# Performance work log

Measured on AMD Instinct MI355X. Metric: run time of the kernel, lower is better.

The kernel has to match this reference:

```python
import jax, jax.numpy as jnp
import numpy as np

# Qwen2 MoE MLP layer: top-k router -> token dispatch -> grouped SwiGLU MLP -> weighted combine.
S, B, H = 2048, 1, 1024      # seq, batch, hidden
E, K, F = 8, 2, 1408         # num_experts, top_k, moe_intermediate (fc1 emits 2*F for SwiGLU)

def setup_inputs() -> dict:
    key = jax.random.key(0)
    k1, k2, k3, k4 = jax.random.split(key, 4)
    return {
        "hidden_states": jax.random.normal(k1, (S, B, H), jnp.float32),
        "router_weight": jax.random.normal(k2, (H, E), jnp.float32) * 0.02,
        "w1": jax.random.normal(k3, (E, H, 2 * F), jnp.float32) * 0.02,  # grouped fc1 (gate|up)
        "w2": jax.random.normal(k4, (E, F, H), jnp.float32) * 0.02,      # grouped fc2
    }

def reference(hidden_states, router_weight, w1, w2):
    s, b, h = hidden_states.shape
    x = hidden_states.reshape(-1, h)                      # [T, H], T = S*B
    logits = x @ router_weight                            # [T, E]
    probs = jax.nn.softmax(logits, axis=-1)
    _, topk_idx = jax.lax.top_k(probs, K)                 # token -> top-k expert ids
    routing_map = jax.nn.one_hot(topk_idx, E, dtype=probs.dtype).sum(axis=1)  # [T, E] 0/1 mask
    local_probs = probs * routing_map                     # combine weights, zero off-topk
    # Grouped SwiGLU MLP. The torch module permutes tokens to expert groups and runs
    # grouped GEMMs; with static shapes the equivalent math is dense-per-expert with
    # the routing mask folded into the combine weights (identical output).
    y = jnp.einsum('th,ehf->tef', x, w1)                  # [T, E, 2F]
    y1, y2 = jnp.split(y, 2, axis=-1)
    g = jax.nn.silu(y1) * y2                              # swiglu, [T, E, F]
    o = jnp.einsum('tef,efh->teh', g, w2)                 # [T, E, H]
    out = jnp.einsum('teh,te->th', o, local_probs)        # unpermute + prob-weighted combine
    return out.reshape(s, b, h)
```

## Files before the change

kernel.cpp:

```cpp
#include <hip/hip_runtime.h>
#include <hip/hip_bf16.h>
#include <stdint.h>

#define T_TOK 2048
#define HD    1024
#define NE    8
#define FD    1408
#define F2D   2816
#define HP    1056
#define OP    1056

#define BM 128
#define BK 32
#define MAXMT 40
#define MAXSLOTS 5120
#define FC1_NT 22
#define FC2_NT 16
#define FC1_NWG (FC1_NT * MAXMT)
#define FC2_NWG (FC2_NT * MAXMT)
#define FC1_CHUNK 110
#define FC2_CHUNK 80

typedef __attribute__((ext_vector_type(8))) short bf16x8;
typedef __attribute__((ext_vector_type(4))) float f32x4;
typedef __attribute__((ext_vector_type(2))) int i32x2;

__device__ __forceinline__ unsigned short f2bf(float f) {
  unsigned int u = __float_as_uint(f);
  u += 0x7FFFu + ((u >> 16) & 1u);
  return (unsigned short)(u >> 16);
}

#define GLL16(gp, lp) __builtin_amdgcn_global_load_lds( \
    (const __attribute__((address_space(1))) void*)(gp), \
    (__attribute__((address_space(3))) void*)(lp), 16, 0, 0)

#define LDS_OFF(p) ((unsigned)(uintptr_t)(__attribute__((address_space(3))) const unsigned short*)(p))

__device__ __forceinline__ void tr_issue(unsigned a, i32x2& lo, i32x2& hi) {
  asm volatile("ds_read_b64_tr_b16 %0, %2\n\t"
               "ds_read_b64_tr_b16 %1, %2 offset:512"
               : "=&v"(lo), "=&v"(hi)
               : "v"(a)
               : "memory");
}
__device__ __forceinline__ bf16x8 tr_pack(i32x2 lo, i32x2 hi) {
  union { i32x2 v; short s[4]; } a, b;
  a.v = lo; b.v = hi;
  bf16x8 f;
  f[0] = a.s[0]; f[1] = a.s[1]; f[2] = a.s[2]; f[3] = a.s[3];
  f[4] = b.s[0]; f[5] = b.s[1]; f[6] = b.s[2]; f[7] = b.s[3];
  return f;
}

__global__ __launch_bounds__(256) void k_router(
    const float* __restrict__ x, const float* __restrict__ rw,
    unsigned short* __restrict__ xbf, int* __restrict__ ctrl,
    int* __restrict__ tok_e, float* __restrict__ tok_p)
{
  const int lane = threadIdx.x & 63;
  const int t = blockIdx.x * 4 + (threadIdx.x >> 6);
  const float* xr = x + (size_t)t * HD;

  float part[8];
#pragma unroll
  for (int e = 0; e < 8; ++e) part[e] = 0.f;

#pragma unroll
  for (int i = 0; i < 16; ++i) {
    const int h = i * 64 + lane;
    const float xv = xr[h];
    xbf[(size_t)t * HP + h] = f2bf(xv);
    const float4* rwr = reinterpret_cast<const float4*>(rw + (size_t)h * 8);
    float4 a = rwr[0], bb = rwr[1];
    part[0] += xv * a.x; part[1] += xv * a.y; part[2] += xv * a.z; part[3] += xv * a.w;
    part[4] += xv * bb.x; part[5] += xv * bb.y; part[6] += xv * bb.z; part[7] += xv * bb.w;
  }
#pragma unroll
  for (int e = 0; e < 8; ++e) {
    float v = part[e];
#pragma unroll
    for (int d = 32; d; d >>= 1) v += __shfl_xor(v, d, 64);
    part[e] = v;
  }
  float m = part[0];
#pragma unroll
  for (int e = 1; e < 8; ++e) m = fmaxf(m, part[e]);
  float p[8], s = 0.f;
#pragma unroll
  for (int e = 0; e < 8; ++e) { p[e] = __expf(part[e] - m); s += p[e]; }
  const float inv = 1.f / s;
#pragma unroll
  for (int e = 0; e < 8; ++e) p[e] *= inv;

  int e0 = 0; float p0 = p[0];
#pragma unroll
  for (int e = 1; e < 8; ++e) if (p[e] > p0) { p0 = p[e]; e0 = e; }
  int e1 = -1; float p1 = -1.f;
#pragma unroll
  for (int e = 0; e < 8; ++e) if (e != e0 && p[e] > p1) { p1 = p[e]; e1 = e; }

  if (lane == 0) {
    tok_e[t * 2 + 0] = e0; tok_e[t * 2 + 1] = e1;
    tok_p[t * 2 + 0] = p0; tok_p[t * 2 + 1] = p1;
    atomicAdd(&ctrl[e0], 1);
    atomicAdd(&ctrl[e1], 1);
  }
}

__global__ __launch_bounds__(256) void k_offsets(
    int* __restrict__ ctrl, int* __restrict__ stok, float* __restrict__ sp,
    int* __restrict__ widmt1, int* __restrict__ widmt2)
{
  __shared__ int soff[8], scnt[8], sFirst[8], sNmt[8], sTake[8];
  __shared__ int sSpill;
  if (threadIdx.x == 0) {
    int o = 0, nm = 0, spill = 0;
    for (int e = 0; e < 8; ++e) {
      ctrl[16 + e] = o; soff[e] = o; scnt[e] = ctrl[e];
      const int n = ctrl[e];
      const int nmt = (n + BM - 1) / BM;
      sFirst[e] = nm; sNmt[e] = nmt; sTake[e] = nmt < 5 ? nmt : 5;
      if (nmt > 5) spill = 1;
      for (int j = 0; j < nmt; ++j) { ctrl[24 + nm] = e; ctrl[64 + nm] = o + j * BM; ++nm; }
      o += nmt * BM;
    }
    for (int i = nm; i < MAXMT; ++i) ctrl[24 + i] = -1;
    sSpill = spill;
  }
  __syncthreads();
  for (int i = threadIdx.x; i < FC1_NWG; i += 256) {
    const int e = i / FC1_CHUNK, r = i % FC1_CHUNK;
    const int j = r / FC1_NT, n = r % FC1_NT;
    widmt1[i] = (j < sTake[e]) ? (sFirst[e] + j) * 32 + n : -1;
  }
  for (int i = threadIdx.x; i < FC2_NWG; i += 256) {
    const int e = i / FC2_CHUNK, r = i % FC2_CHUNK;
    const int j = r / FC2_NT, n = r % FC2_NT;
    widmt2[i] = (j < sTake[e]) ? (sFirst[e] + j) * 32 + n : -1;
  }
  __syncthreads();
  if (sSpill && threadIdx.x == 0) {
    int cur = 0;
    for (int e = 0; e < 8; ++e)
      for (int j = 5; j < sNmt[e]; ++j)
        for (int n = 0; n < FC1_NT; ++n) {
          while (widmt1[cur] != -1) ++cur;
          widmt1[cur] = (sFirst[e] + j) * 32 + n;
        }
    cur = 0;
    for (int e = 0; e < 8; ++e)
      for (int j = 5; j < sNmt[e]; ++j)
        for (int n = 0; n < FC2_NT; ++n) {
          while (widmt2[cur] != -1) ++cur;
          widmt2[cur] = (sFirst[e] + j) * 32 + n;
        }
  }
  for (int e = 0; e < 8; ++e) {
    const int n = scnt[e], o = soff[e];
    const int padEnd = (n + BM - 1) / BM * BM;
    for (int j = n + (int)threadIdx.x; j < padEnd; j += 256) {
      stok[o + j] = 0; sp[o + j] = 0.f;
    }
  }
}

__global__ __launch_bounds__(256) void k_scatter(
    int* __restrict__ ctrl, const int* __restrict__ tok_e,
    const float* __restrict__ tok_p, int* __restrict__ stok,
    float* __restrict__ sp, int* __restrict__ tslot)
{
  const int t = blockIdx.x * 256 + threadIdx.x;
#pragma unroll
  for (int k = 0; k < 2; ++k) {
    const int e = tok_e[t * 2 + k];
    const float pp = tok_p[t * 2 + k];
    const int pos = atomicAdd(&ctrl[8 + e], 1);
    const int slot = ctrl[16 + e] + pos;
    stok[slot] = t; sp[slot] = pp;
    tslot[t * 2 + k] = slot;
  }
}

__global__ __launch_bounds__(256) void k_fc1(
    const unsigned short* __restrict__ xbf,
    const float* __restrict__ w1,
    const int* __restrict__ ctrl,
    const int* __restrict__ stok,
    const float* __restrict__ sp,
    const int* __restrict__ widmt1,
    unsigned short* __restrict__ g)
{
  const int bid = blockIdx.x;
  const int wid = (bid & 7) * FC1_CHUNK + (bid >> 3);
  const int packed = widmt1[wid];
  if (packed < 0) return;
  const int mt = packed >> 5;
  const int e = ctrl[24 + mt];
  const int rowbase = ctrl[64 + mt];
  const int n0 = (packed & 31) * 64;

  __shared__ unsigned short sA[3][BM * BK];
  __shared__ unsigned short sB1[3][64 * BK];
  __shared__ unsigned short sB2[3][64 * BK];

  const int tid = threadIdx.x;
  const int lane = tid & 63;
  const int wave = tid >> 6;
  const int wm = wave >> 1, wn = wave & 1;

  const int schunk = (lane & 3) ^ ((lane >> 3) & 3);
  const unsigned short* aSrc[2];
#pragma unroll
  for (int t4 = 0; t4 < 2; ++t4) {
    const int row = (t4 * 4 + wave) * 16 + (lane >> 2);
    const int tok = stok[rowbase + row];
    aSrc[t4] = xbf + (size_t)tok * HP + schunk * 8;
  }

  const int kdec = wave * 8 + ((lane >> 5) << 2) + ((lane >> 1) & 3);
  const int ndec = ((lane >> 3) & 3) * 16 + (lane & 1) * 8;
  const float* b1SrcF = w1 + ((size_t)e * HD + kdec) * F2D + n0 + ndec;
  const float* b2SrcF = b1SrcF + FD;

  const int c = lane >> 4;
  int aoff[4];
#pragma unroll
  for (int m = 0; m < 4; ++m) {
    const int row = wm * 64 + m * 16 + (lane & 15);
    aoff[m] = row * 32 + ((c ^ ((row >> 1) & 3)) << 3);
  }
  const unsigned trlane = (lane & 15) * 8 + (lane >> 4) * 1024;
  unsigned trb[2];
#pragma unroll
  for (int n = 0; n < 2; ++n) trb[n] = trlane + (wn * 2 + n) * 128;
  const unsigned b1base = LDS_OFF(&sB1[0][0]);
  const unsigned b2base = LDS_OFF(&sB2[0][0]);

  const f32x4 zero = {0.f, 0.f, 0.f, 0.f};
  f32x4 acc1[4][2], acc2[4][2];
#pragma unroll
  for (int m = 0; m < 4; ++m)
#pragma unroll
    for (int n = 0; n < 2; ++n) { acc1[m][n] = zero; acc2[m][n] = zero; }

  float b1r0[8], b2r0[8], b1r1[8], b2r1[8];

#define FC1_BLOAD(KT, R1, R2) do {                                  \
    const float* _p1 = b1SrcF + (size_t)(KT) * BK * F2D;            \
    const float* _p2 = b2SrcF + (size_t)(KT) * BK * F2D;            \
    *(float4*)&R1[0] = *(const float4*)_p1;                         \
    *(float4*)&R1[4] = *(const float4*)(_p1 + 4);                   \
    *(float4*)&R2[0] = *(const float4*)_p2;                         \
    *(float4*)&R2[4] = *(const float4*)(_p2 + 4);                   \
  } while (0)

#define FC1_BWRITE(BUF, R1, R2) do {                                \
    bf16x8 _v1, _v2;                                                \
    for (int _j = 0; _j < 8; ++_j) {                                \
      _v1[_j] = (short)f2bf(R1[_j]);                                \
      _v2[_j] = (short)f2bf(R2[_j]);                                \
    }                                                               \
    *(bf16x8*)&sB1[BUF][wave * 512 + lane * 8] = _v1;               \
    *(bf16x8*)&sB2[BUF][wave * 512 + lane * 8] = _v2;               \
  } while (0)

#define FC1_ASTAGE(BUF, KT) do {                                    \
    for (int _t4 = 0; _t4 < 2; ++_t4)                               \
      GLL16(aSrc[_t4] + (size_t)(KT) * BK, &sA[BUF][(_t4 * 4 + wave) * 512]); \
  } while (0)

  const int NSTEP = HD / BK;
  FC1_BLOAD(0, b1r0, b2r0);
  __builtin_amdgcn_sched_barrier(0);
  asm volatile("s_waitcnt vmcnt(0)" ::: "memory");
  FC1_BWRITE(0, b1r0, b2r0);
  __builtin_amdgcn_sched_barrier(0);
  FC1_BLOAD(1, b1r1, b2r1);
  __builtin_amdgcn_sched_barrier(0);
  FC1_ASTAGE(0, 0);
  __builtin_amdgcn_sched_barrier(0);
  FC1_BLOAD(2, b1r0, b2r0);
  __builtin_amdgcn_sched_barrier(0);
  FC1_ASTAGE(1, 1);
  __builtin_amdgcn_sched_barrier(0);
  asm volatile("s_waitcnt lgkmcnt(0)" ::: "memory");

#define FC1_STEP(T, R1, R2) do {                                             \
    const int _t = (T);                                                      \
    if (_t < NSTEP - 2)      { asm volatile("s_waitcnt vmcnt(6)" ::: "memory"); } \
    else if (_t == NSTEP - 2){ asm volatile("s_waitcnt vmcnt(2)" ::: "memory"); } \
    else                     { asm volatile("s_waitcnt vmcnt(0)" ::: "memory"); } \
    __builtin_amdgcn_s_barrier();                                            \
    __builtin_amdgcn_sched_barrier(0);                                       \
    int _bnext = bsel + 1; if (_bnext >= 3) _bnext -= 3;                     \
    int _bn2 = bsel + 2; if (_bn2 >= 3) _bn2 -= 3;                           \
    if (_t + 1 < NSTEP) FC1_BWRITE(_bnext, R1, R2);                          \
    __builtin_amdgcn_sched_barrier(0);                                       \
    if (_t + 3 < NSTEP) FC1_BLOAD(_t + 3, R1, R2);                           \
    __builtin_amdgcn_sched_barrier(0);                                       \
    if (_t + 2 < NSTEP) FC1_ASTAGE(_bn2, _t + 2);                            \
    __builtin_amdgcn_sched_barrier(0);                                       \
    bf16x8 _af[4];                                                           \
    for (int _m = 0; _m < 4; ++_m)                                           \
      _af[_m] = *(const bf16x8*)&sA[bsel][aoff[_m]];                         \
    i32x2 _q1lo[2], _q1hi[2], _q2lo[2], _q2hi[2];                            \
    for (int _n = 0; _n < 2; ++_n) {                                         \
      tr_issue(b1base + bsel * 4096 + trb[_n], _q1lo[_n], _q1hi[_n]);        \
      tr_issue(b2base + bsel * 4096 + trb[_n], _q2lo[_n], _q2hi[_n]);        \
    }                                                                        \
    asm volatile("s_waitcnt lgkmcnt(0)" ::: "memory");                       \
    __builtin_amdgcn_sched_barrier(0);                                       \
    bf16x8 _b1f[2], _b2f[2];                                                 \
    for (int _n = 0; _n < 2; ++_n) {                                         \
      _b1f[_n] = tr_pack(_q1lo[_n], _q1hi[_n]);                              \
      _b2f[_n] = tr_pack(_q2lo[_n], _q2hi[_n]);                              \
    }                                                                        \
    __builtin_amdgcn_s_setprio(1);                                           \
    for (int _m = 0; _m < 4; ++_m)                                           \
      for (int _n = 0; _n < 2; ++_n) {                                       \
        acc1[_m][_n] = __builtin_amdgcn_mfma_f32_16x16x32_bf16(_af[_m], _b1f[_n], acc1[_m][_n], 0, 0, 0); \
        acc2[_m][_n] = __builtin_amdgcn_mfma_f32_16x16x32_bf16(_af[_m], _b2f[_n], acc2[_m][_n], 0, 0, 0); \
      }                                                                      \
    __builtin_amdgcn_s_setprio(0);                                           \
  } while (0)

  int bsel = 0;
  for (int tt = 0; tt < NSTEP; tt += 2) {
    FC1_STEP(tt, b1r1, b2r1);
    bsel = bsel + 1 == 3 ? 0 : bsel + 1;
    FC1_STEP(tt + 1, b1r0, b2r0);
    bsel = bsel + 1 == 3 ? 0 : bsel + 1;
  }

  float prv[4][4];
#pragma unroll
  for (int m = 0; m < 4; ++m)
#pragma unroll
    for (int r = 0; r < 4; ++r)
      prv[m][r] = sp[rowbase + wm * 64 + m * 16 + (lane >> 4) * 4 + r];

#pragma unroll
  for (int m = 0; m < 4; ++m) {
    const int rb = rowbase + wm * 64 + m * 16 + (lane >> 4) * 4;
#pragma unroll
    for (int n = 0; n < 2; ++n) {
      const int col = n0 + wn * 32 + n * 16 + (lane & 15);
#pragma unroll
      for (int r = 0; r < 4; ++r) {
        const float y1 = acc1[m][n][r];
        const float y2 = acc2[m][n][r];
        const float gv = y1 / (1.f + __expf(-y1)) * y2 * prv[m][r];
        g[(size_t)(rb + r) * FD + col] = f2bf(gv);
      }
    }
  }
}

__global__ __launch_bounds__(256) void k_fc2(
    const unsigned short* __restrict__ g,
    const float* __restrict__ w2,
    const int* __restrict__ ctrl,
    const int* __restrict__ widmt2,
    float* __restrict__ o)
{
  const int bid = blockIdx.x;
  const int wid = (bid & 7) * FC2_CHUNK + (bid >> 3);
  const int packed = widmt2[wid];
  if (packed < 0) return;
  const int mt = packed >> 5;
  const int e = ctrl[24 + mt];
  const int rowbase = ctrl[64 + mt];
  const int n0 = (packed & 31) * 64;

  __shared__ unsigned short sA[3][BM * BK];
  __shared__ unsigned short sB[3][64 * BK];

  const int tid = threadIdx.x;
  const int lane = tid & 63;
  const int wave = tid >> 6;
  const int wm = wave >> 1, wn = wave & 1;

  const int schunk = (lane & 3) ^ ((lane >> 3) & 3);
  const unsigned short* aSrc[2];
#pragma unroll
  for (int t4 = 0; t4 < 2; ++t4) {
    const int row = (t4 * 4 + wave) * 16 + (lane >> 2);
    aSrc[t4] = g + (size_t)(rowbase + row) * FD + schunk * 8;
  }

  const int kdec = wave * 8 + ((lane >> 5) << 2) + ((lane >> 1) & 3);
  const int ndec = ((lane >> 3) & 3) * 16 + (lane & 1) * 8;
  const float* bSrcF = w2 + ((size_t)e * FD + kdec) * HD + n0 + ndec;

  const int c = lane >> 4;
  int aoff[4];
#pragma unroll
  for (int m = 0; m < 4; ++m) {
    const int row = wm * 64 + m * 16 + (lane & 15);
    aoff[m] = row * 32 + ((c ^ ((row >> 1) & 3)) << 3);
  }
  const unsigned trlane = (lane & 15) * 8 + (lane >> 4) * 1024;
  unsigned trb[2];
#pragma unroll
  for (int n = 0; n < 2; ++n) trb[n] = trlane + (wn * 2 + n) * 128;
  const unsigned bbase = LDS_OFF(&sB[0][0]);

  const f32x4 zero = {0.f, 0.f, 0.f, 0.f};
  f32x4 acc[4][2];
#pragma unroll
  for (int m = 0; m < 4; ++m)
#pragma unroll
    for (int n = 0; n < 2; ++n) acc[m][n] = zero;

  float br0[8], br1[8];

#define FC2_BLOAD(KT, R) do {                                       \
    const float* _p = bSrcF + (size_t)(KT) * BK * HD;               \
    *(float4*)&R[0] = *(const float4*)_p;                           \
    *(float4*)&R[4] = *(const float4*)(_p + 4);                     \
  } while (0)

#define FC2_BWRITE(BUF, R) do {                                     \
    bf16x8 _v;                                                      \
    for (int _j = 0; _j < 8; ++_j) _v[_j] = (short)f2bf(R[_j]);     \
    *(bf16x8*)&sB[BUF][wave * 512 + lane * 8] = _v;                 \
  } while (0)

#define FC2_ASTAGE(BUF, KT) do {                                    \
    for (int _t4 = 0; _t4 < 2; ++_t4)                               \
      GLL16(aSrc[_t4] + (size_t)(KT) * BK, &sA[BUF][(_t4 * 4 + wave) * 512]); \
  } while (0)

  const int NSTEP = FD / BK;
  FC2_BLOAD(0, br0);
  __builtin_amdgcn_sched_barrier(0);
  asm volatile("s_waitcnt vmcnt(0)" ::: "memory");
  FC2_BWRITE(0, br0);
  __builtin_amdgcn_sched_barrier(0);
  FC2_BLOAD(1, br1);
  __builtin_amdgcn_sched_barrier(0);
  FC2_ASTAGE(0, 0);
  __builtin_amdgcn_sched_barrier(0);
  FC2_BLOAD(2, br0);
  __builtin_amdgcn_sched_barrier(0);
  FC2_ASTAGE(1, 1);
  __builtin_amdgcn_sched_barrier(0);
  asm volatile("s_waitcnt lgkmcnt(0)" ::: "memory");

#define FC2_STEP(T, R) do {                                                  \
    const int _t = (T);                                                      \
    if (_t < NSTEP - 2)      { asm volatile("s_waitcnt vmcnt(4)" ::: "memory"); } \
    else if (_t == NSTEP - 2){ asm volatile("s_waitcnt vmcnt(2)" ::: "memory"); } \
    else                     { asm volatile("s_waitcnt vmcnt(0)" ::: "memory"); } \
    __builtin_amdgcn_s_barrier();                                            \
    __builtin_amdgcn_sched_barrier(0);                                       \
    int _bnext = bsel + 1; if (_bnext >= 3) _bnext -= 3;                     \
    int _bn2 = bsel + 2; if (_bn2 >= 3) _bn2 -= 3;                           \
    if (_t + 1 < NSTEP) FC2_BWRITE(_bnext, R);                               \
    __builtin_amdgcn_sched_barrier(0);                                       \
    if (_t + 3 < NSTEP) FC2_BLOAD(_t + 3, R);                                \
    __builtin_amdgcn_sched_barrier(0);                                       \
    if (_t + 2 < NSTEP) FC2_ASTAGE(_bn2, _t + 2);                            \
    __builtin_amdgcn_sched_barrier(0);                                       \
    bf16x8 _af[4];                                                           \
    for (int _m = 0; _m < 4; ++_m)                                           \
      _af[_m] = *(const bf16x8*)&sA[bsel][aoff[_m]];                         \
    i32x2 _qlo[2], _qhi[2];                                                  \
    for (int _n = 0; _n < 2; ++_n)                                           \
      tr_issue(bbase + bsel * 4096 + trb[_n], _qlo[_n], _qhi[_n]);           \
    asm volatile("s_waitcnt lgkmcnt(0)" ::: "memory");                       \
    __builtin_amdgcn_sched_barrier(0);                                       \
    bf16x8 _bf[2];                                                           \
    for (int _n = 0; _n < 2; ++_n) _bf[_n] = tr_pack(_qlo[_n], _qhi[_n]);    \
    __builtin_amdgcn_s_setprio(1);                                           \
    for (int _m = 0; _m < 4; ++_m)                                           \
      for (int _n = 0; _n < 2; ++_n)                                         \
        acc[_m][_n] = __builtin_amdgcn_mfma_f32_16x16x32_bf16(_af[_m], _bf[_n], acc[_m][_n], 0, 0, 0); \
    __builtin_amdgcn_s_setprio(0);                                           \
  } while (0)

  int bsel = 0;
  for (int tt = 0; tt < NSTEP; tt += 2) {
    FC2_STEP(tt, br1);
    bsel = bsel + 1 == 3 ? 0 : bsel + 1;
    FC2_STEP(tt + 1, br0);
    bsel = bsel + 1 == 3 ? 0 : bsel + 1;
  }

#pragma unroll
  for (int m = 0; m < 4; ++m) {
    const int rb = rowbase + wm * 64 + m * 16 + (lane >> 4) * 4;
#pragma unroll
    for (int n = 0; n < 2; ++n) {
      const int col = n0 + wn * 32 + n * 16 + (lane & 15);
#pragma unroll
      for (int r = 0; r < 4; ++r)
        o[(size_t)(rb + r) * OP + col] = acc[m][n][r];
    }
  }
}

__global__ __launch_bounds__(256) void k_combine(
    const float* __restrict__ o, const int* __restrict__ tslot,
    float* __restrict__ out)
{
  const int t = blockIdx.x;
  const int c4 = threadIdx.x;
  const int sA = tslot[t * 2], sB = tslot[t * 2 + 1];
  const float4 a = reinterpret_cast<const float4*>(o + (size_t)sA * OP)[c4];
  const float4 b = reinterpret_cast<const float4*>(o + (size_t)sB * OP)[c4];
  float4 r;
  r.x = a.x + b.x; r.y = a.y + b.y; r.z = a.z + b.z; r.w = a.w + b.w;
  reinterpret_cast<float4*>(out)[(size_t)t * 256 + c4] = r;
}

extern "C" void kernel_launch(void* const* d_in, const int* in_sizes, int n_in,
                              void* d_out, int out_size, void* d_ws, size_t ws_size,
                              hipStream_t stream)
{
  const float* x  = (const float*)d_in[0];
  const float* rw = (const float*)d_in[1];
  const float* w1 = (const float*)d_in[2];
  const float* w2 = (const float*)d_in[3];
  float* out = (float*)d_out;
  char* ws = (char*)d_ws;

  int*   ctrl   = (int*)(ws + 0);
  int*   tok_e  = (int*)(ws + 1024);
  float* tok_p  = (float*)(ws + 17408);
  int*   stok   = (int*)(ws + 33792);
  float* sp     = (float*)(ws + 54272);
  int*   tslot  = (int*)(ws + 74752);
  int*   widmt1 = (int*)(ws + 91136);
  int*   widmt2 = (int*)(ws + 94656);
  unsigned short* xbf = (unsigned short*)(ws + 97280);
  unsigned short* g   = (unsigned short*)(ws + 4422656);
  float*          o   = (float*)(ws + 18840576);

  hipMemsetAsync(ws, 0, 1024, stream);

  k_router<<<T_TOK / 4, 256, 0, stream>>>(x, rw, xbf, ctrl, tok_e, tok_p);
  k_offsets<<<1, 256, 0, stream>>>(ctrl, stok, sp, widmt1, widmt2);
  k_scatter<<<T_TOK / 256, 256, 0, stream>>>(ctrl, tok_e, tok_p, stok, sp, tslot);
  k_fc1<<<FC1_NWG, 256, 0, stream>>>(xbf, w1, ctrl, stok, sp, widmt1, g);
  k_fc2<<<FC2_NWG, 256, 0, stream>>>(g, w2, ctrl, widmt2, o);
  k_combine<<<T_TOK, 256, 0, stream>>>(o, tslot, out);
}
```

Before: 198.0 us.

## Fold scatter into offsets kernel, use packed bf16 converts, split MFMA/LDS waits

Merges the token scatter into the single-block offsets kernel, using shared-memory atomics instead of global ones and removing one kernel launch. Replaces the per-element float-to-bf16 conversion of weight tiles with packed v_cvt_pk_bf16_f32 inline asm. Splits the LDS transpose reads so the first column's MFMAs start after a partial lgkmcnt wait, overlapping LDS latency with compute. The scatter now runs on a single workgroup, which serializes 4096 atomic placements, and the inline asm changes bf16 rounding to the hardware conversion mode.

Result: faster. 170.7 us (-13.8%).

```diff
diff --git a/kernel.cpp b/kernel.cpp
--- a/kernel.cpp
+++ b/kernel.cpp
@@ -109,15 +109,17 @@
 }
 
 __global__ __launch_bounds__(256) void k_offsets(
-    int* __restrict__ ctrl, int* __restrict__ stok, float* __restrict__ sp,
+    int* __restrict__ ctrl, const int* __restrict__ tok_e,
+    const float* __restrict__ tok_p, int* __restrict__ stok,
+    float* __restrict__ sp, int* __restrict__ tslot,
     int* __restrict__ widmt1, int* __restrict__ widmt2)
 {
-  __shared__ int soff[8], scnt[8], sFirst[8], sNmt[8], sTake[8];
+  __shared__ int soff[8], scnt[8], sFirst[8], sNmt[8], sTake[8], sCur[8];
   __shared__ int sSpill;
   if (threadIdx.x == 0) {
     int o = 0, nm = 0, spill = 0;
     for (int e = 0; e < 8; ++e) {
-      ctrl[16 + e] = o; soff[e] = o; scnt[e] = ctrl[e];
+      ctrl[16 + e] = o; soff[e] = o; scnt[e] = ctrl[e]; sCur[e] = 0;
       const int n = ctrl[e];
       const int nmt = (n + BM - 1) / BM;
       sFirst[e] = nm; sNmt[e] = nmt; sTake[e] = nmt < 5 ? nmt : 5;
@@ -163,22 +165,15 @@
       stok[o + j] = 0; sp[o + j] = 0.f;
     }
   }
-}
-
-__global__ __launch_bounds__(256) void k_scatter(
-    int* __restrict__ ctrl, const int* __restrict__ tok_e,
-    const float* __restrict__ tok_p, int* __restrict__ stok,
-    float* __restrict__ sp, int* __restrict__ tslot)
-{
-  const int t = blockIdx.x * 256 + threadIdx.x;
-#pragma unroll
-  for (int k = 0; k < 2; ++k) {
-    const int e = tok_e[t * 2 + k];
-    const float pp = tok_p[t * 2 + k];
-    const int pos = atomicAdd(&ctrl[8 + e], 1);
-    const int slot = ctrl[16 + e] + pos;
-    stok[slot] = t; sp[slot] = pp;
-    tslot[t * 2 + k] = slot;
+  for (int i = threadIdx.x; i < T_TOK; i += 256) {
+#pragma unroll
+    for (int k = 0; k < 2; ++k) {
+      const int e = tok_e[i * 2 + k];
+      const int pos = atomicAdd(&sCur[e], 1);
+      const int slot = soff[e] + pos;
+      stok[slot] = i; sp[slot] = tok_p[i * 2 + k];
+      tslot[i * 2 + k] = slot;
+    }
   }
 }
 
@@ -256,13 +251,19 @@
   } while (0)
 
 #define FC1_BWRITE(BUF, R1, R2) do {                                \
-    bf16x8 _v1, _v2;                                                \
-    for (int _j = 0; _j < 8; ++_j) {                                \
-      _v1[_j] = (short)f2bf(R1[_j]);                                \
-      _v2[_j] = (short)f2bf(R2[_j]);                                \
-    }                                                               \
-    *(bf16x8*)&sB1[BUF][wave * 512 + lane * 8] = _v1;               \
-    *(bf16x8*)&sB2[BUF][wave * 512 + lane * 8] = _v2;               \
+    unsigned _a0,_a1,_a2,_a3,_c0,_c1,_c2,_c3;                       \
+    asm("v_cvt_pk_bf16_f32 %0, %1, %2" : "=v"(_a0) : "v"(R1[0]), "v"(R1[1])); \
+    asm("v_cvt_pk_bf16_f32 %0, %1, %2" : "=v"(_a1) : "v"(R1[2]), "v"(R1[3])); \
+    asm("v_cvt_pk_bf16_f32 %0, %1, %2" : "=v"(_a2) : "v"(R1[4]), "v"(R1[5])); \
+    asm("v_cvt_pk_bf16_f32 %0, %1, %2" : "=v"(_a3) : "v"(R1[6]), "v"(R1[7])); \
+    asm("v_cvt_pk_bf16_f32 %0, %1, %2" : "=v"(_c0) : "v"(R2[0]), "v"(R2[1])); \
+    asm("v_cvt_pk_bf16_f32 %0, %1, %2" : "=v"(_c1) : "v"(R2[2]), "v"(R2[3])); \
+    asm("v_cvt_pk_bf16_f32 %0, %1, %2" : "=v"(_c2) : "v"(R2[4]), "v"(R2[5])); \
+    asm("v_cvt_pk_bf16_f32 %0, %1, %2" : "=v"(_c3) : "v"(R2[6]), "v"(R2[7])); \
+    uint4 _u1 = make_uint4(_a0,_a1,_a2,_a3);                        \
+    uint4 _u2 = make_uint4(_c0,_c1,_c2,_c3);                        \
+    *(uint4*)&sB1[BUF][wave * 512 + lane * 8] = _u1;                \
+    *(uint4*)&sB2[BUF][wave * 512 + lane * 8] = _u2;                \
   } while (0)
 
 #define FC1_ASTAGE(BUF, KT) do {                                    \
@@ -304,24 +305,32 @@
     bf16x8 _af[4];                                                           \
     for (int _m = 0; _m < 4; ++_m)                                           \
       _af[_m] = *(const bf16x8*)&sA[bsel][aoff[_m]];                         \
+    __builtin_amdgcn_sched_barrier(0);                                       \
     i32x2 _q1lo[2], _q1hi[2], _q2lo[2], _q2hi[2];                            \
-    for (int _n = 0; _n < 2; ++_n) {                                         \
-      tr_issue(b1base + bsel * 4096 + trb[_n], _q1lo[_n], _q1hi[_n]);        \
-      tr_issue(b2base + bsel * 4096 + trb[_n], _q2lo[_n], _q2hi[_n]);        \
+    tr_issue(b1base + bsel * 4096 + trb[0], _q1lo[0], _q1hi[0]);             \
+    tr_issue(b2base + bsel * 4096 + trb[0], _q2lo[0], _q2hi[0]);             \
+    __builtin_amdgcn_sched_barrier(0);                                       \
+    tr_issue(b1base + bsel * 4096 + trb[1], _q1lo[1], _q1hi[1]);             \
+    tr_issue(b2base + bsel * 4096 + trb[1], _q2lo[1], _q2hi[1]);             \
+    asm volatile("s_waitcnt lgkmcnt(4)" ::: "memory");                       \
+    __builtin_amdgcn_sched_barrier(0);                                       \
+    bf16x8 _b1f0 = tr_pack(_q1lo[0], _q1hi[0]);                              \
+    bf16x8 _b2f0 = tr_pack(_q2lo[0], _q2hi[0]);                              \
+    __builtin_amdgcn_s_setprio(1);                                           \
+    for (int _m = 0; _m < 4; ++_m) {                                         \
+      acc1[_m][0] = __builtin_amdgcn_mfma_f32_16x16x32_bf16(_af[_m], _b1f0, acc1[_m][0], 0, 0, 0); \
+      acc2[_m][0] = __builtin_amdgcn_mfma_f32_16x16x32_bf16(_af[_m], _b2f0, acc2[_m][0], 0, 0, 0); \
     }                                                                        \
+    __builtin_amdgcn_s_setprio(0);                                           \
     asm volatile("s_waitcnt lgkmcnt(0)" ::: "memory");                       \
     __builtin_amdgcn_sched_barrier(0);                                       \
-    bf16x8 _b1f[2], _b2f[2];                                                 \
-    for (int _n = 0; _n < 2; ++_n) {                                         \
-      _b1f[_n] = tr_pack(_q1lo[_n], _q1hi[_n]);                              \
-      _b2f[_n] = tr_pack(_q2lo[_n], _q2hi[_n]);                              \
+    bf16x8 _b1f1 = tr_pack(_q1lo[1], _q1hi[1]);                              \
+    bf16x8 _b2f1 = tr_pack(_q2lo[1], _q2hi[1]);                              \
+    __builtin_amdgcn_s_setprio(1);                                           \
+    for (int _m = 0; _m < 4; ++_m) {                                         \
+      acc1[_m][1] = __builtin_amdgcn_mfma_f32_16x16x32_bf16(_af[_m], _b1f1, acc1[_m][1], 0, 0, 0); \
+      acc2[_m][1] = __builtin_amdgcn_mfma_f32_16x16x32_bf16(_af[_m], _b2f1, acc2[_m][1], 0, 0, 0); \
     }                                                                        \
-    __builtin_amdgcn_s_setprio(1);                                           \
-    for (int _m = 0; _m < 4; ++_m)                                           \
-      for (int _n = 0; _n < 2; ++_n) {                                       \
-        acc1[_m][_n] = __builtin_amdgcn_mfma_f32_16x16x32_bf16(_af[_m], _b1f[_n], acc1[_m][_n], 0, 0, 0); \
-        acc2[_m][_n] = __builtin_amdgcn_mfma_f32_16x16x32_bf16(_af[_m], _b2f[_n], acc2[_m][_n], 0, 0, 0); \
-      }                                                                      \
     __builtin_amdgcn_s_setprio(0);                                           \
   } while (0)
 
@@ -422,9 +431,13 @@
   } while (0)
 
 #define FC2_BWRITE(BUF, R) do {                                     \
-    bf16x8 _v;                                                      \
-    for (int _j = 0; _j < 8; ++_j) _v[_j] = (short)f2bf(R[_j]);     \
-    *(bf16x8*)&sB[BUF][wave * 512 + lane * 8] = _v;                 \
+    unsigned _a0,_a1,_a2,_a3;                                       \
+    asm("v_cvt_pk_bf16_f32 %0, %1, %2" : "=v"(_a0) : "v"(R[0]), "v"(R[1])); \
+    asm("v_cvt_pk_bf16_f32 %0, %1, %2" : "=v"(_a1) : "v"(R[2]), "v"(R[3])); \
+    asm("v_cvt_pk_bf16_f32 %0, %1, %2" : "=v"(_a2) : "v"(R[4]), "v"(R[5])); \
+    asm("v_cvt_pk_bf16_f32 %0, %1, %2" : "=v"(_a3) : "v"(R[6]), "v"(R[7])); \
+    uint4 _u = make_uint4(_a0,_a1,_a2,_a3);                         \
+    *(uint4*)&sB[BUF][wave * 512 + lane * 8] = _u;                  \
   } while (0)
 
 #define FC2_ASTAGE(BUF, KT) do {                                    \
@@ -466,17 +479,24 @@
     bf16x8 _af[4];                                                           \
     for (int _m = 0; _m < 4; ++_m)                                           \
       _af[_m] = *(const bf16x8*)&sA[bsel][aoff[_m]];                         \
+    __builtin_amdgcn_sched_barrier(0);                                       \
     i32x2 _qlo[2], _qhi[2];                                                  \
-    for (int _n = 0; _n < 2; ++_n)                                           \
-      tr_issue(bbase + bsel * 4096 + trb[_n], _qlo[_n], _qhi[_n]);           \
-    asm volatile("s_waitcnt lgkmcnt(0)" ::: "memory");                       \
-    __builtin_amdgcn_sched_barrier(0);                                       \
-    bf16x8 _bf[2];                                                           \
-    for (int _n = 0; _n < 2; ++_n) _bf[_n] = tr_pack(_qlo[_n], _qhi[_n]);    \
+    tr_issue(bbase + bsel * 4096 + trb[0], _qlo[0], _qhi[0]);                \
+    __builtin_amdgcn_sched_barrier(0);                                       \
+    tr_issue(bbase + bsel * 4096 + trb[1], _qlo[1], _qhi[1]);                \
+    asm volatile("s_waitcnt lgkmcnt(2)" ::: "memory");                       \
+    __builtin_amdgcn_sched_barrier(0);                                       \
+    bf16x8 _bf0 = tr_pack(_qlo[0], _qhi[0]);                                 \
     __builtin_amdgcn_s_setprio(1);                                           \
     for (int _m = 0; _m < 4; ++_m)                                           \
-      for (int _n = 0; _n < 2; ++_n)                                         \
-        acc[_m][_n] = __builtin_amdgcn_mfma_f32_16x16x32_bf16(_af[_m], _bf[_n], acc[_m][_n], 0, 0, 0); \
+      acc[_m][0] = __builtin_amdgcn_mfma_f32_16x16x32_bf16(_af[_m], _bf0, acc[_m][0], 0, 0, 0); \
+    __builtin_amdgcn_s_setprio(0);                                           \
+    asm volatile("s_waitcnt lgkmcnt(0)" ::: "memory");                       \
+    __builtin_amdgcn_sched_barrier(0);                                       \
+    bf16x8 _bf1 = tr_pack(_qlo[1], _qhi[1]);                                 \
+    __builtin_amdgcn_s_setprio(1);                                           \
+    for (int _m = 0; _m < 4; ++_m)                                           \
+      acc[_m][1] = __builtin_amdgcn_mfma_f32_16x16x32_bf16(_af[_m], _bf1, acc[_m][1], 0, 0, 0); \
     __builtin_amdgcn_s_setprio(0);                                           \
   } while (0)
 
@@ -541,8 +561,7 @@
   hipMemsetAsync(ws, 0, 1024, stream);
 
   k_router<<<T_TOK / 4, 256, 0, stream>>>(x, rw, xbf, ctrl, tok_e, tok_p);
-  k_offsets<<<1, 256, 0, stream>>>(ctrl, stok, sp, widmt1, widmt2);
-  k_scatter<<<T_TOK / 256, 256, 0, stream>>>(ctrl, tok_e, tok_p, stok, sp, tslot);
+  k_offsets<<<1, 256, 0, stream>>>(ctrl, tok_e, tok_p, stok, sp, tslot, widmt1, widmt2);
   k_fc1<<<FC1_NWG, 256, 0, stream>>>(xbf, w1, ctrl, stok, sp, widmt1, g);
   k_fc2<<<FC2_NWG, 256, 0, stream>>>(g, w2, ctrl, widmt2, o);
   k_combine<<<T_TOK, 256, 0, stream>>>(o, tslot, out);
```
